# Performance work log

Hardware: AMD Instinct MI355X
Metric: run time of the kernel (lower is better)

Reference implementation:

```python
import jax, jax.numpy as jnp
import numpy as np

STRIDE = (4, 4)
MASK = (17, 17)
G_MEAN = 85.384
G_STD = 53.798
LEV = 5  # len(bins)
EPS = 1e-8
_BINS = np.array([0.0, 0.5, G_MEAN - G_STD, G_MEAN, G_MEAN + G_STD], dtype=np.float32)
_DISTS = [1, 2, 4]
_THETAS = [0.0, np.pi / 4, np.pi / 2, 3 * np.pi / 4]
# skimage greycomatrix offsets: (row, col) = (round(sin(t)*d), round(cos(t)*d)), dist-major
OFFSETS = [(int(round(np.sin(t) * d)), int(round(np.cos(t) * d))) for d in _DISTS for t in _THETAS]


def setup_inputs():
    key = jax.random.key(0)
    x = jax.random.uniform(key, (8, 1, 512, 512), dtype=jnp.float32) * 255.0
    return {"inputs": x}


def _sliding_windows(x):
    B, C, H, W = x.shape
    nx = (H - MASK[0]) // STRIDE[0] + 1
    ny = (W - MASK[1]) // STRIDE[1] + 1
    rows = (jnp.arange(nx) * STRIDE[0])[:, None] + jnp.arange(MASK[0])  # (nx, Mx)
    cols = (jnp.arange(ny) * STRIDE[1])[:, None] + jnp.arange(MASK[1])  # (ny, My)
    w = x[:, :, rows]              # (B, C, nx, Mx, W)
    w = w[:, :, :, :, cols]        # (B, C, nx, Mx, ny, My)
    return jnp.transpose(w, (0, 1, 2, 4, 3, 5))  # (B, C, nx, ny, Mx, My)


def _statistics(w):
    m = w.mean(axis=(-2, -1))
    s = w.std(axis=(-2, -1))
    mx = w.max(axis=(-2, -1))
    mn = w.min(axis=(-2, -1))
    # Faithful to original: mean is rescaled in-place BEFORE being used in max/min stats
    m = m / G_MEAN
    s = s / G_STD
    mx = (mx - m) / G_STD
    mn = (m - mn) / G_STD
    return jnp.concatenate([m, s, mx, mn], axis=1)  # (B, 4*C, nx, ny)


def _glcm(qf, dr, dc):
    # qf: (Wn, Mx, My) int32 -> normalized symmetric GLCM (Wn, LEV, LEV)
    Mx, My = qf.shape[-2:]
    if dc >= 0:
        a = qf[:, :Mx - dr, :My - dc]
        b = qf[:, dr:, dc:]
    else:
        a = qf[:, :Mx - dr, -dc:]
        b = qf[:, dr:, :My + dc]
    Wn = qf.shape[0]
    code = (a * LEV + b).reshape(Wn, -1)
    flat = (jnp.arange(Wn, dtype=jnp.int32)[:, None] * (LEV * LEV) + code).reshape(-1)
    cnt = jax.ops.segment_sum(jnp.ones(flat.shape, jnp.float32), flat, num_segments=Wn * LEV * LEV)
    G = cnt.reshape(Wn, LEV, LEV)
    G = G + jnp.swapaxes(G, -1, -2)  # symmetric=True
    return G / jnp.sum(G, axis=(-2, -1), keepdims=True)  # normed=True


def _hist_glcm_features(q):
    # q: (B, C, nx, ny, Mx, My) int32 -> (B, 64, nx, ny) (C must be 1)
    B, C, nx, ny, Mx, My = q.shape
    qf = q.reshape(-1, Mx, My)
    Wn = qf.shape[0]
    G = jnp.stack([_glcm(qf, dr, dc) for dr, dc in OFFSETS], axis=1)  # (Wn, 12, L, L)

    I = jnp.arange(LEV, dtype=jnp.float32)
    d2 = (I[:, None] - I[None, :]) ** 2
    contrast = jnp.einsum('wkij,ij->wk', G, d2)
    homogeneity = jnp.einsum('wkij,ij->wk', G, 1.0 / (1.0 + d2))
    energy = jnp.sqrt(jnp.sum(G * G, axis=(-2, -1)))
    Pi = G.sum(axis=-1)   # (Wn, 12, L)
    Pj = G.sum(axis=-2)
    mu_i = jnp.sum(I * Pi, axis=-1)
    mu_j = jnp.sum(I * Pj, axis=-1)
    di = I[None, None, :] - mu_i[..., None]
    dj = I[None, None, :] - mu_j[..., None]
    std_i = jnp.sqrt(jnp.sum(Pi * di * di, axis=-1))
    std_j = jnp.sqrt(jnp.sum(Pj * dj * dj, axis=-1))
    cov = jnp.einsum('wkij,wki,wkj->wk', G, di, dj)
    denom = std_i * std_j
    correlation = jnp.where(denom < 1e-15, 1.0, cov / jnp.maximum(denom, 1e-30))
    entropy = -jnp.sum(G * jnp.log2(G + EPS), axis=(-2, -1))  # (Wn, 12)

    qv = qf.reshape(Wn, -1)
    cnts = jnp.stack([jnp.sum(qv == k, axis=-1) for k in range(1, LEV)], axis=-1).astype(jnp.float32)
    tot = cnts.sum(axis=-1, keepdims=True)
    hist = jnp.where(tot > 0, cnts / jnp.maximum(tot, 1.0), 0.0)  # (Wn, LEV-1)

    feat = jnp.concatenate([hist, contrast, homogeneity, energy, correlation, entropy], axis=-1)
    feat = feat.reshape(B, C, nx, ny, -1)
    return jnp.transpose(feat, (0, 4, 2, 3, 1))[..., 0]  # (B, 64, nx, ny)


def reference(inputs):
    w = _sliding_windows(inputs)                                   # (B,C,nx,ny,17,17)
    stat = _statistics(w)                                          # (B,4,nx,ny)
    q = (jnp.digitize(w, jnp.asarray(_BINS)) - 1).astype(jnp.int32)
    hg = _hist_glcm_features(q)                                    # (B,64,nx,ny)
    feats = jnp.concatenate([stat, hg], axis=1)                    # (B,68,nx,ny)
    return jnp.mean(feats, axis=(-2, -1))                          # (B,68)
```

## Files before the change

kernel.cpp:

```cpp
#include <hip/hip_runtime.h>


#define G_MEAN_F 85.384f
#define G_STD_F  53.798f
#define MASK_WS_BYTES (8u * 512u * 36u * 8u)

__device__ constexpr int LO15[15] = {0,0,0,0,0,1,1,1,1,2,2,2,3,3,4};
__device__ constexpr int HI15[15] = {0,1,2,3,4,1,2,3,4,2,3,4,3,4,4};

__device__ __forceinline__ float wred(float v) {
#pragma unroll
  for (int m = 32; m; m >>= 1) v += __shfl_xor(v, m, 64);
  return v;
}

__device__ __forceinline__ void load_row(const unsigned long long* mrow, int ly4, unsigned m[5]) {
  unsigned long long a = mrow[0], b = mrow[1], c = mrow[2], d = mrow[3];
  m[1] = (unsigned)(a >> ly4) & 0x1FFFFu;
  m[2] = (unsigned)(b >> ly4) & 0x1FFFFu;
  m[3] = (unsigned)(c >> ly4) & 0x1FFFFu;
  m[4] = (unsigned)(d >> ly4) & 0x1FFFFu;
  m[0] = 0x1FFFFu & ~(m[1] | m[2] | m[3] | m[4]);
}

template<int DC>
__device__ __forceinline__ void updoff(unsigned cnt[15], const unsigned a[5], const unsigned b[5]) {
  unsigned as[5], bs[5];
#pragma unroll
  for (int v = 0; v < 5; ++v) {
    as[v] = (DC < 0) ? (a[v] >> (-DC)) : a[v];
    bs[v] = (DC > 0) ? (b[v] >> DC) : b[v];
  }
#pragma unroll
  for (int u = 0; u < 15; ++u) {
    const int i = LO15[u], j = HI15[u];
    unsigned t = as[i] & bs[j];
    if (i != j) t |= as[j] & bs[i];
    cnt[u] += __popc(t);
  }
}

__device__ __forceinline__ void feat5(const unsigned cnt[15], float Np,
                                      float& con, float& hom, float& ene,
                                      float& corr, float& ent) {
  const float invN = 1.0f / Np;
  const float inv2N = 0.5f / Np;
  con = 0.0f; hom = 0.0f; ent = 0.0f;
  float eac = 0.0f;
  float P[5] = {0, 0, 0, 0, 0};
#pragma unroll
  for (int u = 0; u < 15; ++u) {
    const int lo = LO15[u], hi = HI15[u];
    const float m = (float)cnt[u];
    const float d2 = (float)((hi - lo) * (hi - lo));
    con += m * d2;
    hom += m * (1.0f / (1.0f + d2));
    if (lo == hi) {
      eac += m * m;
      P[lo] += 2.0f * m;
      float g = m * invN;
      ent -= g * __log2f(g + 1e-8f);
    } else {
      eac += 0.5f * m * m;
      P[lo] += m; P[hi] += m;
      float g = m * inv2N;
      ent -= 2.0f * g * __log2f(g + 1e-8f);
    }
  }
  con *= invN;
  hom *= invN;
  ene = sqrtf(eac) * invN;
  float mu = 0.0f;
#pragma unroll
  for (int i = 0; i < 5; ++i) { P[i] *= inv2N; mu += (float)i * P[i]; }
  float s2 = 0.0f;
#pragma unroll
  for (int i = 0; i < 5; ++i) { float d = (float)i - mu; s2 = fmaf(P[i] * d, d, s2); }
  float denom = s2;
  float cov = 0.0f;
#pragma unroll
  for (int u = 0; u < 15; ++u)
    cov += ((float)cnt[u] * invN) * ((float)LO15[u] - mu) * ((float)HI15[u] - mu);
  corr = (denom < 1e-15f) ? 1.0f : cov / fmaxf(denom, 1e-30f);
}

__device__ __forceinline__ void emit2(const unsigned c1[15], const unsigned c2[15], float Np,
                                      bool v1, bool v2, float* pt0, int k0, int k1) {
  float con1, hom1, ene1, cor1, ent1, con2, hom2, ene2, cor2, ent2;
  feat5(c1, Np, con1, hom1, ene1, cor1, ent1);
  feat5(c2, Np, con2, hom2, ene2, cor2, ent2);
  if (!v1) { con1 = 0; hom1 = 0; ene1 = 0; cor1 = 0; ent1 = 0; }
  if (!v2) { con2 = 0; hom2 = 0; ene2 = 0; cor2 = 0; ent2 = 0; }
  float con = wred(con1 + con2), hom = wred(hom1 + hom2), ene = wred(ene1 + ene2);
  float cor = wred(cor1 + cor2), ent = wred(ent1 + ent2);
  if ((threadIdx.x & 63) == 0) {
    const float s = 1.0f / 15376.0f;
    pt0[(8 + k0) * 128] = con * s;
    pt0[(20 + k0) * 128] = hom * s;
    pt0[(32 + k0) * 128] = ene * s;
    pt0[(44 + k0) * 128] = cor * s;
    pt0[(56 + k0) * 128] = ent * s;
    if (k1 >= 0) {
      pt0[(8 + k1) * 128] = con * s;
      pt0[(20 + k1) * 128] = hom * s;
      pt0[(32 + k1) * 128] = ene * s;
      pt0[(44 + k1) * 128] = cor * s;
      pt0[(56 + k1) * 128] = ent * s;
    }
  }
}

template<int DR>
__device__ __forceinline__ void shiftbuf(unsigned buf[][5], const unsigned c[5]) {
#pragma unroll
  for (int i = 0; i < DR - 1; ++i)
#pragma unroll
    for (int v = 0; v < 5; ++v) buf[i][v] = buf[i + 1][v];
#pragma unroll
  for (int v = 0; v < 5; ++v) buf[DR - 1][v] = c[v];
}

template<int DR, int DC>
__device__ __forceinline__ void glcm_pass(const unsigned long long* mk, int s, int ly4,
                                          float Np, bool v1, bool v2, float* pt0,
                                          int k0, int k1) {
  unsigned A[15], S[15], B[15];
#pragma unroll
  for (int u = 0; u < 15; ++u) { A[u] = 0; S[u] = 0; B[u] = 0; }
  unsigned c[5];
  if (DR == 0) {
#pragma unroll 1
    for (int R = 0; R < 4; ++R)  { load_row(mk + (s + R) * 5, ly4, c); updoff<DC>(A, c, c); }
#pragma unroll 1
    for (int R = 4; R < 17; ++R) { load_row(mk + (s + R) * 5, ly4, c); updoff<DC>(S, c, c); }
#pragma unroll 1
    for (int R = 17; R < 21; ++R){ load_row(mk + (s + R) * 5, ly4, c); updoff<DC>(B, c, c); }
  } else {
    unsigned buf[DR > 0 ? DR : 1][5];
#pragma unroll
    for (int i = 0; i < DR; ++i) load_row(mk + (s + i) * 5, ly4, buf[i]);
#pragma unroll 1
    for (int R = 0; R < 4; ++R) {
      load_row(mk + (s + R + DR) * 5, ly4, c);
      updoff<DC>(A, buf[0], c);
      shiftbuf<DR>(buf, c);
    }
#pragma unroll 1
    for (int R = 4; R < 17 - DR; ++R) {
      load_row(mk + (s + R + DR) * 5, ly4, c);
      updoff<DC>(S, buf[0], c);
      shiftbuf<DR>(buf, c);
    }
#pragma unroll 1
    for (int R = 17 - DR; R < 21 - DR; ++R) {
      load_row(mk + (s + R + DR) * 5, ly4, c);
      updoff<DC>(B, buf[0], c);
      shiftbuf<DR>(buf, c);
    }
  }
#pragma unroll
  for (int u = 0; u < 15; ++u) { A[u] += S[u]; B[u] += S[u]; }
  emit2(A, B, Np, v1, v2, pt0, k0, k1);
}

__global__ __launch_bounds__(64)
void mask_build_kernel(const float* __restrict__ x, unsigned long long* __restrict__ mg) {
  const int lane = threadIdx.x;
  const int r = blockIdx.x;
  const int b = blockIdx.y;
  const float* xr = x + ((size_t)b * 512 + r) * 512;
  unsigned long long* mr = mg + ((size_t)b * 512 + r) * 36;

  const float T1 = 0.5f;
  const float T2 = (float)(85.384 - 53.798);
  const float T3 = 85.384f;
  const float T4 = (float)(85.384 + 53.798);

#pragma unroll 1
  for (int seg = 0; seg < 8; ++seg) {
    float xv = xr[seg * 64 + lane];
    int q = (int)(xv >= T1) + (int)(xv >= T2) + (int)(xv >= T3) + (int)(xv >= T4);
    unsigned long long b1 = __ballot(q == 1);
    unsigned long long b2 = __ballot(q == 2);
    unsigned long long b3 = __ballot(q == 3);
    unsigned long long b4 = __ballot(q == 4);
    if (lane < 4) {
      unsigned long long bv = (lane == 0) ? b1 : (lane == 1) ? b2 : (lane == 2) ? b3 : b4;
      mr[seg * 4 + lane] = bv;
    }
  }
  if (lane < 4) mr[32 + lane] = 0;
}

__global__ __launch_bounds__(128)
void glcm_feat_kernel(const float* __restrict__ x,
                      const unsigned long long* __restrict__ mg,
                      float* __restrict__ part) {
  __shared__ unsigned long long masks[77 * 5];

  const int tid = threadIdx.x;
  const int lane = tid & 63;
  const int wid = tid >> 6;
  const int u = blockIdx.x >> 4;
  const int ty = blockIdx.x & 15;
  const int tx = blockIdx.y;
  const int b = blockIdx.z;
  const int px0 = tx * 64;
  const int py0 = ty * 32;
  const float* xb = x + (size_t)b * 512 * 512;

  const int s0 = py0 >> 6;
  const int sh = py0 & 63;
  const unsigned long long* mgb = mg + (size_t)b * 512 * 36;
#pragma unroll 1
  for (int t = tid; t < 77 * 4; t += 128) {
    int row = t >> 2, lev = t & 3;
    int gr = px0 + row; if (gr > 511) gr = 511;
    const unsigned long long* p = mgb + (size_t)gr * 36 + s0 * 4 + lev;
    unsigned long long w0 = p[0];
    unsigned long long w1 = p[4];
    masks[row * 5 + lev] = sh ? ((w0 >> 32) | (w1 << 32)) : w0;
  }
  __syncthreads();

  const int lxp = lane >> 3, ly = lane & 7;
  const int wx1 = tx * 16 + 2 * lxp;
  const int wy = ty * 8 + ly;
  const bool vy = (wy < 124);
  const bool v1 = (wx1 < 124) && vy;
  const bool v2 = (wx1 + 1 < 124) && vy;
  const int s = 8 * lxp;
  const int ly4 = ly * 4;
  const int tile = tx * 16 + ty;
  float* pt0 = part + (size_t)b * 68 * 128 + tile;

  if (u == 0) {
    if (wid == 0) {
      int sp = px0 + s; if (sp > 488) sp = 488;
      int c0 = py0 + ly4; if (c0 > 492) c0 = 492;
      const float* fw = xb + (size_t)sp * 512 + c0;
      float sA = 0, qA = 0, sS = 0, qS = 0, sB = 0, qB = 0;
      float mxA = -1e30f, mnA = 1e30f, mxS = -1e30f, mnS = 1e30f, mxB = -1e30f, mnB = 1e30f;
#pragma unroll 1
      for (int r = 0; r < 21; ++r) {
        const float* p = fw + r * 512;
        const float4* p4 = (const float4*)p;
        float rs = 0, rq = 0, rmx = -1e30f, rmn = 1e30f;
#pragma unroll
        for (int w = 0; w < 4; ++w) {
          float4 f = p4[w];
          rs += f.x; rq = fmaf(f.x, f.x, rq); rmx = fmaxf(rmx, f.x); rmn = fminf(rmn, f.x);
          rs += f.y; rq = fmaf(f.y, f.y, rq); rmx = fmaxf(rmx, f.y); rmn = fminf(rmn, f.y);
          rs += f.z; rq = fmaf(f.z, f.z, rq); rmx = fmaxf(rmx, f.z); rmn = fminf(rmn, f.z);
          rs += f.w; rq = fmaf(f.w, f.w, rq); rmx = fmaxf(rmx, f.w); rmn = fminf(rmn, f.w);
        }
        float t = p[16];
        rs += t; rq = fmaf(t, t, rq); rmx = fmaxf(rmx, t); rmn = fminf(rmn, t);
        if (r < 4)       { sA += rs; qA += rq; mxA = fmaxf(mxA, rmx); mnA = fminf(mnA, rmn); }
        else if (r < 17) { sS += rs; qS += rq; mxS = fmaxf(mxS, rmx); mnS = fminf(mnS, rmn); }
        else             { sB += rs; qB += rq; mxB = fmaxf(mxB, rmx); mnB = fminf(mnB, rmn); }
      }
      float ch[4][2];
#pragma unroll
      for (int w = 0; w < 2; ++w) {
        float sum = w ? (sS + sB) : (sA + sS);
        float ssq = w ? (qS + qB) : (qA + qS);
        float mx = w ? fmaxf(mxS, mxB) : fmaxf(mxA, mxS);
        float mn = w ? fminf(mnS, mnB) : fminf(mnA, mnS);
        float mean = sum * (1.0f / 289.0f);
        float var = fmaxf(ssq * (1.0f / 289.0f) - mean * mean, 0.0f);
        float fm = mean / G_MEAN_F;
        ch[0][w] = fm;
        ch[1][w] = sqrtf(var) / G_STD_F;
        ch[2][w] = (mx - fm) / G_STD_F;
        ch[3][w] = (fm - mn) / G_STD_F;
      }
#pragma unroll
      for (int c = 0; c < 4; ++c) {
        float f = (v1 ? ch[c][0] : 0.0f) + (v2 ? ch[c][1] : 0.0f);
        f = wred(f);
        if (lane == 0) pt0[c * 128] = f * (1.0f / 15376.0f);
      }
    } else {
      unsigned hA[4] = {0,0,0,0}, hS[4] = {0,0,0,0}, hB[4] = {0,0,0,0};
#pragma unroll 1
      for (int R = 0; R < 21; ++R) {
        unsigned m[5];
        load_row(masks + (s + R) * 5, ly4, m);
        unsigned* h = (R < 4) ? hA : (R < 17) ? hS : hB;
#pragma unroll
        for (int v = 0; v < 4; ++v) h[v] += __popc(m[v + 1]);
      }
      float ch[4][2];
#pragma unroll
      for (int w = 0; w < 2; ++w) {
        unsigned t1 = w ? (hS[0] + hB[0]) : (hA[0] + hS[0]);
        unsigned t2 = w ? (hS[1] + hB[1]) : (hA[1] + hS[1]);
        unsigned t3 = w ? (hS[2] + hB[2]) : (hA[2] + hS[2]);
        unsigned t4 = w ? (hS[3] + hB[3]) : (hA[3] + hS[3]);
        unsigned tot = t1 + t2 + t3 + t4;
        float ti = (tot > 0) ? 1.0f / (float)tot : 0.0f;
        ch[0][w] = (float)t1 * ti;
        ch[1][w] = (float)t2 * ti;
        ch[2][w] = (float)t3 * ti;
        ch[3][w] = (float)t4 * ti;
      }
#pragma unroll
      for (int c = 0; c < 4; ++c) {
        float f = (v1 ? ch[c][0] : 0.0f) + (v2 ? ch[c][1] : 0.0f);
        f = wred(f);
        if (lane == 0) pt0[(4 + c) * 128] = f * (1.0f / 15376.0f);
      }
    }
  } else if (u == 1) {
    if (wid == 0) glcm_pass<0, 1>(masks, s, ly4, 272.0f, v1, v2, pt0, 0, -1);
    else          glcm_pass<1, 0>(masks, s, ly4, 272.0f, v1, v2, pt0, 2, -1);
  } else if (u == 2) {
    if (wid == 0) glcm_pass<0, 2>(masks, s, ly4, 255.0f, v1, v2, pt0, 4, -1);
    else          glcm_pass<1, 1>(masks, s, ly4, 256.0f, v1, v2, pt0, 1, 5);
  } else if (u == 3) {
    if (wid == 0) glcm_pass<0, 4>(masks, s, ly4, 221.0f, v1, v2, pt0, 8, -1);
    else          glcm_pass<1, -1>(masks, s, ly4, 256.0f, v1, v2, pt0, 3, 7);
  } else if (u == 4) {
    if (wid == 0) glcm_pass<2, 0>(masks, s, ly4, 255.0f, v1, v2, pt0, 6, -1);
    else          glcm_pass<3, 3>(masks, s, ly4, 196.0f, v1, v2, pt0, 9, -1);
  } else {
    if (wid == 0) glcm_pass<4, 0>(masks, s, ly4, 221.0f, v1, v2, pt0, 10, -1);
    else          glcm_pass<3, -3>(masks, s, ly4, 196.0f, v1, v2, pt0, 11, -1);
  }
}

__global__ __launch_bounds__(64)
void reduce_kernel(const float* __restrict__ part, float* __restrict__ out) {
  const int ch = blockIdx.x;
  const int b = blockIdx.y;
  const int lane = threadIdx.x;
  const float2* p = (const float2*)(part + ((size_t)b * 68 + ch) * 128);
  float2 f = p[lane];
  float v = f.x + f.y;
  v = wred(v);
  if (lane == 0) out[b * 68 + ch] = v;
}

extern "C" void kernel_launch(void* const* d_in, const int* in_sizes, int n_in,
                              void* d_out, int out_size, void* d_ws, size_t ws_size,
                              hipStream_t stream)
{
  const float* x = (const float*)d_in[0];
  float* out = (float*)d_out;
  unsigned long long* mg = (unsigned long long*)d_ws;
  float* part = (float*)((char*)d_ws + MASK_WS_BYTES);

  mask_build_kernel<<<dim3(512, 8), dim3(64), 0, stream>>>(x, mg);
  glcm_feat_kernel<<<dim3(96, 8, 8), dim3(128), 0, stream>>>(x, mg, part);
  reduce_kernel<<<dim3(68, 8), dim3(64), 0, stream>>>(part, out);
}
```

Baseline: 113.4 us.

## Process four vertically adjacent windows per thread with segmented row sharing

Each thread now covers four overlapping windows instead of two. Rows are split into seven segments whose partial GLCM counts, histograms and statistics are combined, so rows shared between windows are scanned once. Mask rows are pre-shifted into 17-bit shared-memory slices and read with a single uint4 load, which drops the per-row 64-bit shifts. The tile height doubles and the grid's x-tiles halve, which raises register pressure from the 7x15 counters and leaves fewer blocks in flight.

```diff
diff --git a/kernel.cpp b/kernel.cpp
--- a/kernel.cpp
+++ b/kernel.cpp
@@ -14,17 +14,14 @@
   return v;
 }
 
-__device__ __forceinline__ void load_row(const unsigned long long* mrow, int ly4, unsigned m[5]) {
-  unsigned long long a = mrow[0], b = mrow[1], c = mrow[2], d = mrow[3];
-  m[1] = (unsigned)(a >> ly4) & 0x1FFFFu;
-  m[2] = (unsigned)(b >> ly4) & 0x1FFFFu;
-  m[3] = (unsigned)(c >> ly4) & 0x1FFFFu;
-  m[4] = (unsigned)(d >> ly4) & 0x1FFFFu;
+__device__ __forceinline__ void load_sl(const unsigned* sl, int idx, unsigned m[5]) {
+  const uint4 q = *(const uint4*)(sl + idx * 4);
+  m[1] = q.x; m[2] = q.y; m[3] = q.z; m[4] = q.w;
   m[0] = 0x1FFFFu & ~(m[1] | m[2] | m[3] | m[4]);
 }
 
 template<int DC>
-__device__ __forceinline__ void updoff(unsigned cnt[15], const unsigned a[5], const unsigned b[5]) {
+__device__ __forceinline__ void updoff(unsigned* cnt, const unsigned a[5], const unsigned b[5]) {
   unsigned as[5], bs[5];
 #pragma unroll
   for (int v = 0; v < 5; ++v) {
@@ -40,7 +37,28 @@
   }
 }
 
-__device__ __forceinline__ void feat5(const unsigned cnt[15], float Np,
+template<int DR, int DC>
+__device__ __forceinline__ void seg_run(unsigned* cnt, const unsigned* sl, int sly,
+                                        int RB, int RE, unsigned (*buf)[5]) {
+#pragma unroll 1
+  for (int R = RB; R < RE; ++R) {
+    unsigned c[5];
+    load_sl(sl, sly + (R + DR) * 8, c);
+    if constexpr (DR > 0) {
+      updoff<DC>(cnt, buf[0], c);
+#pragma unroll
+      for (int i = 0; i < DR - 1; ++i)
+#pragma unroll
+        for (int v = 0; v < 5; ++v) buf[i][v] = buf[i + 1][v];
+#pragma unroll
+      for (int v = 0; v < 5; ++v) buf[DR - 1][v] = c[v];
+    } else {
+      updoff<DC>(cnt, c, c);
+    }
+  }
+}
+
+__device__ __forceinline__ void feat5(const unsigned* cnt, float Np,
                                       float& con, float& hom, float& ene,
                                       float& corr, float& ent) {
   const float invN = 1.0f / Np;
@@ -84,83 +102,89 @@
   corr = (denom < 1e-15f) ? 1.0f : cov / fmaxf(denom, 1e-30f);
 }
 
-__device__ __forceinline__ void emit2(const unsigned c1[15], const unsigned c2[15], float Np,
-                                      bool v1, bool v2, float* pt0, int k0, int k1) {
-  float con1, hom1, ene1, cor1, ent1, con2, hom2, ene2, cor2, ent2;
-  feat5(c1, Np, con1, hom1, ene1, cor1, ent1);
-  feat5(c2, Np, con2, hom2, ene2, cor2, ent2);
-  if (!v1) { con1 = 0; hom1 = 0; ene1 = 0; cor1 = 0; ent1 = 0; }
-  if (!v2) { con2 = 0; hom2 = 0; ene2 = 0; cor2 = 0; ent2 = 0; }
-  float con = wred(con1 + con2), hom = wred(hom1 + hom2), ene = wred(ene1 + ene2);
-  float cor = wred(cor1 + cor2), ent = wred(ent1 + ent2);
+template<int DR, int DC>
+__device__ void glcm4(const unsigned* sl, int sly, bool v0, bool v1, bool v2, bool v3,
+                      float Np, float* pt0, int k0, int k1) {
+  unsigned A[7][15];
+#pragma unroll
+  for (int p = 0; p < 7; ++p)
+#pragma unroll
+    for (int u = 0; u < 15; ++u) A[p][u] = 0;
+
+  unsigned buf[DR > 0 ? DR : 1][5];
+  if constexpr (DR > 0) {
+#pragma unroll
+    for (int i = 0; i < DR; ++i) load_sl(sl, sly + i * 8, buf[i]);
+  }
+  seg_run<DR, DC>(A[0], sl, sly, 0, 4, buf);
+  seg_run<DR, DC>(A[1], sl, sly, 4, 8, buf);
+  seg_run<DR, DC>(A[2], sl, sly, 8, 12, buf);
+  seg_run<DR, DC>(A[3], sl, sly, 12, 17 - DR, buf);
+  seg_run<DR, DC>(A[4], sl, sly, 17 - DR, 21 - DR, buf);
+  seg_run<DR, DC>(A[5], sl, sly, 21 - DR, 25 - DR, buf);
+  seg_run<DR, DC>(A[6], sl, sly, 25 - DR, 29 - DR, buf);
+
+#pragma unroll
+  for (int u = 0; u < 15; ++u) {
+    A[0][u] += A[1][u] + A[2][u] + A[3][u];
+    A[1][u] += A[2][u] + A[3][u] + A[4][u];
+    A[2][u] += A[3][u] + A[4][u] + A[5][u];
+    A[3][u] += A[4][u] + A[5][u] + A[6][u];
+  }
+  float con = 0, hom = 0, ene = 0, cor = 0, ent = 0;
+  const bool vv[4] = {v0, v1, v2, v3};
+#pragma unroll
+  for (int w = 0; w < 4; ++w) {
+    float c5, h5, e5, r5, t5;
+    feat5(A[w], Np, c5, h5, e5, r5, t5);
+    if (vv[w]) { con += c5; hom += h5; ene += e5; cor += r5; ent += t5; }
+  }
+  con = wred(con); hom = wred(hom); ene = wred(ene); cor = wred(cor); ent = wred(ent);
   if ((threadIdx.x & 63) == 0) {
     const float s = 1.0f / 15376.0f;
-    pt0[(8 + k0) * 128] = con * s;
-    pt0[(20 + k0) * 128] = hom * s;
-    pt0[(32 + k0) * 128] = ene * s;
-    pt0[(44 + k0) * 128] = cor * s;
-    pt0[(56 + k0) * 128] = ent * s;
+    pt0[(8 + k0) * 64] = con * s;
+    pt0[(20 + k0) * 64] = hom * s;
+    pt0[(32 + k0) * 64] = ene * s;
+    pt0[(44 + k0) * 64] = cor * s;
+    pt0[(56 + k0) * 64] = ent * s;
     if (k1 >= 0) {
-      pt0[(8 + k1) * 128] = con * s;
-      pt0[(20 + k1) * 128] = hom * s;
-      pt0[(32 + k1) * 128] = ene * s;
-      pt0[(44 + k1) * 128] = cor * s;
-      pt0[(56 + k1) * 128] = ent * s;
-    }
-  }
-}
-
-template<int DR>
-__device__ __forceinline__ void shiftbuf(unsigned buf[][5], const unsigned c[5]) {
-#pragma unroll
-  for (int i = 0; i < DR - 1; ++i)
-#pragma unroll
-    for (int v = 0; v < 5; ++v) buf[i][v] = buf[i + 1][v];
-#pragma unroll
-  for (int v = 0; v < 5; ++v) buf[DR - 1][v] = c[v];
-}
-
-template<int DR, int DC>
-__device__ __forceinline__ void glcm_pass(const unsigned long long* mk, int s, int ly4,
-                                          float Np, bool v1, bool v2, float* pt0,
-                                          int k0, int k1) {
-  unsigned A[15], S[15], B[15];
-#pragma unroll
-  for (int u = 0; u < 15; ++u) { A[u] = 0; S[u] = 0; B[u] = 0; }
-  unsigned c[5];
-  if (DR == 0) {
-#pragma unroll 1
-    for (int R = 0; R < 4; ++R)  { load_row(mk + (s + R) * 5, ly4, c); updoff<DC>(A, c, c); }
-#pragma unroll 1
-    for (int R = 4; R < 17; ++R) { load_row(mk + (s + R) * 5, ly4, c); updoff<DC>(S, c, c); }
-#pragma unroll 1
-    for (int R = 17; R < 21; ++R){ load_row(mk + (s + R) * 5, ly4, c); updoff<DC>(B, c, c); }
-  } else {
-    unsigned buf[DR > 0 ? DR : 1][5];
-#pragma unroll
-    for (int i = 0; i < DR; ++i) load_row(mk + (s + i) * 5, ly4, buf[i]);
-#pragma unroll 1
-    for (int R = 0; R < 4; ++R) {
-      load_row(mk + (s + R + DR) * 5, ly4, c);
-      updoff<DC>(A, buf[0], c);
-      shiftbuf<DR>(buf, c);
-    }
-#pragma unroll 1
-    for (int R = 4; R < 17 - DR; ++R) {
-      load_row(mk + (s + R + DR) * 5, ly4, c);
-      updoff<DC>(S, buf[0], c);
-      shiftbuf<DR>(buf, c);
-    }
-#pragma unroll 1
-    for (int R = 17 - DR; R < 21 - DR; ++R) {
-      load_row(mk + (s + R + DR) * 5, ly4, c);
-      updoff<DC>(B, buf[0], c);
-      shiftbuf<DR>(buf, c);
-    }
-  }
-#pragma unroll
-  for (int u = 0; u < 15; ++u) { A[u] += S[u]; B[u] += S[u]; }
-  emit2(A, B, Np, v1, v2, pt0, k0, k1);
+      pt0[(8 + k1) * 64] = con * s;
+      pt0[(20 + k1) * 64] = hom * s;
+      pt0[(32 + k1) * 64] = ene * s;
+      pt0[(44 + k1) * 64] = cor * s;
+      pt0[(56 + k1) * 64] = ent * s;
+    }
+  }
+}
+
+__device__ __forceinline__ void stat_rows(const float* fw, int RB, int RE,
+                                          float& sm, float& sq, float& mx, float& mn) {
+#pragma unroll 1
+  for (int r = RB; r < RE; ++r) {
+    const float* p = fw + r * 512;
+    const float4* p4 = (const float4*)p;
+    float rs = 0, rq = 0, rmx = -1e30f, rmn = 1e30f;
+#pragma unroll
+    for (int w = 0; w < 4; ++w) {
+      float4 f = p4[w];
+      rs += f.x; rq = fmaf(f.x, f.x, rq); rmx = fmaxf(rmx, f.x); rmn = fminf(rmn, f.x);
+      rs += f.y; rq = fmaf(f.y, f.y, rq); rmx = fmaxf(rmx, f.y); rmn = fminf(rmn, f.y);
+      rs += f.z; rq = fmaf(f.z, f.z, rq); rmx = fmaxf(rmx, f.z); rmn = fminf(rmn, f.z);
+      rs += f.w; rq = fmaf(f.w, f.w, rq); rmx = fmaxf(rmx, f.w); rmn = fminf(rmn, f.w);
+    }
+    float t = p[16];
+    rs += t; rq = fmaf(t, t, rq); rmx = fmaxf(rmx, t); rmn = fminf(rmn, t);
+    sm += rs; sq += rq; mx = fmaxf(mx, rmx); mn = fminf(mn, rmn);
+  }
+}
+
+__device__ __forceinline__ void hist_rows(const unsigned* sl, int sly, int RB, int RE,
+                                          unsigned* h) {
+#pragma unroll 1
+  for (int R = RB; R < RE; ++R) {
+    const uint4 q = *(const uint4*)(sl + (sly + R * 8) * 4);
+    h[0] += __popc(q.x); h[1] += __popc(q.y); h[2] += __popc(q.z); h[3] += __popc(q.w);
+  }
 }
 
 __global__ __launch_bounds__(64)
@@ -196,7 +220,7 @@
 void glcm_feat_kernel(const float* __restrict__ x,
                       const unsigned long long* __restrict__ mg,
                       float* __restrict__ part) {
-  __shared__ unsigned long long masks[77 * 5];
+  __shared__ __align__(16) unsigned sl[141 * 8 * 4];
 
   const int tid = threadIdx.x;
   const int lane = tid & 63;
@@ -205,128 +229,129 @@
   const int ty = blockIdx.x & 15;
   const int tx = blockIdx.y;
   const int b = blockIdx.z;
-  const int px0 = tx * 64;
+  const int px0 = tx * 128;
   const int py0 = ty * 32;
   const float* xb = x + (size_t)b * 512 * 512;
 
   const int s0 = py0 >> 6;
   const int sh = py0 & 63;
-  const unsigned long long* mgb = mg + (size_t)b * 512 * 36;
-#pragma unroll 1
-  for (int t = tid; t < 77 * 4; t += 128) {
-    int row = t >> 2, lev = t & 3;
+  const unsigned long long* mgb = mg + (size_t)b * 512 * 36 + s0 * 4;
+#pragma unroll 1
+  for (int t = tid; t < 141 * 8; t += 128) {
+    const int row = t >> 3, ly = t & 7;
     int gr = px0 + row; if (gr > 511) gr = 511;
-    const unsigned long long* p = mgb + (size_t)gr * 36 + s0 * 4 + lev;
-    unsigned long long w0 = p[0];
-    unsigned long long w1 = p[4];
-    masks[row * 5 + lev] = sh ? ((w0 >> 32) | (w1 << 32)) : w0;
+    const unsigned long long* p = mgb + (size_t)gr * 36;
+    unsigned sv[4];
+#pragma unroll
+    for (int lev = 0; lev < 4; ++lev) {
+      unsigned long long cmb = p[lev];
+      if (sh) cmb = (cmb >> 32) | (p[4 + lev] << 32);
+      sv[lev] = (unsigned)(cmb >> (4 * ly)) & 0x1FFFFu;
+    }
+    *(uint4*)(sl + t * 4) = make_uint4(sv[0], sv[1], sv[2], sv[3]);
   }
   __syncthreads();
 
   const int lxp = lane >> 3, ly = lane & 7;
-  const int wx1 = tx * 16 + 2 * lxp;
+  const int wxb = tx * 32 + 4 * lxp;
   const int wy = ty * 8 + ly;
   const bool vy = (wy < 124);
-  const bool v1 = (wx1 < 124) && vy;
-  const bool v2 = (wx1 + 1 < 124) && vy;
-  const int s = 8 * lxp;
-  const int ly4 = ly * 4;
+  const bool v0 = vy && (wxb < 124);
+  const bool v1 = vy && (wxb + 1 < 124);
+  const bool v2 = vy && (wxb + 2 < 124);
+  const bool v3 = vy && (wxb + 3 < 124);
+  const int s = 16 * lxp;
+  const int sly = s * 8 + ly;
   const int tile = tx * 16 + ty;
-  float* pt0 = part + (size_t)b * 68 * 128 + tile;
+  float* pt0 = part + (size_t)b * 68 * 64 + tile;
 
   if (u == 0) {
     if (wid == 0) {
-      int sp = px0 + s; if (sp > 488) sp = 488;
-      int c0 = py0 + ly4; if (c0 > 492) c0 = 492;
+      int sp = px0 + s; if (sp > 483) sp = 483;
+      int c0 = py0 + 4 * ly; if (c0 > 492) c0 = 492;
       const float* fw = xb + (size_t)sp * 512 + c0;
-      float sA = 0, qA = 0, sS = 0, qS = 0, sB = 0, qB = 0;
-      float mxA = -1e30f, mnA = 1e30f, mxS = -1e30f, mnS = 1e30f, mxB = -1e30f, mnB = 1e30f;
-#pragma unroll 1
-      for (int r = 0; r < 21; ++r) {
-        const float* p = fw + r * 512;
-        const float4* p4 = (const float4*)p;
-        float rs = 0, rq = 0, rmx = -1e30f, rmn = 1e30f;
-#pragma unroll
-        for (int w = 0; w < 4; ++w) {
-          float4 f = p4[w];
-          rs += f.x; rq = fmaf(f.x, f.x, rq); rmx = fmaxf(rmx, f.x); rmn = fminf(rmn, f.x);
-          rs += f.y; rq = fmaf(f.y, f.y, rq); rmx = fmaxf(rmx, f.y); rmn = fminf(rmn, f.y);
-          rs += f.z; rq = fmaf(f.z, f.z, rq); rmx = fmaxf(rmx, f.z); rmn = fminf(rmn, f.z);
-          rs += f.w; rq = fmaf(f.w, f.w, rq); rmx = fmaxf(rmx, f.w); rmn = fminf(rmn, f.w);
-        }
-        float t = p[16];
-        rs += t; rq = fmaf(t, t, rq); rmx = fmaxf(rmx, t); rmn = fminf(rmn, t);
-        if (r < 4)       { sA += rs; qA += rq; mxA = fmaxf(mxA, rmx); mnA = fminf(mnA, rmn); }
-        else if (r < 17) { sS += rs; qS += rq; mxS = fmaxf(mxS, rmx); mnS = fminf(mnS, rmn); }
-        else             { sB += rs; qB += rq; mxB = fmaxf(mxB, rmx); mnB = fminf(mnB, rmn); }
-      }
-      float ch[4][2];
-#pragma unroll
-      for (int w = 0; w < 2; ++w) {
-        float sum = w ? (sS + sB) : (sA + sS);
-        float ssq = w ? (qS + qB) : (qA + qS);
-        float mx = w ? fmaxf(mxS, mxB) : fmaxf(mxA, mxS);
-        float mn = w ? fminf(mnS, mnB) : fminf(mnA, mnS);
+      float sm[7], sq[7], mx[7], mn[7];
+#pragma unroll
+      for (int p = 0; p < 7; ++p) { sm[p] = 0; sq[p] = 0; mx[p] = -1e30f; mn[p] = 1e30f; }
+      stat_rows(fw, 0, 4, sm[0], sq[0], mx[0], mn[0]);
+      stat_rows(fw, 4, 8, sm[1], sq[1], mx[1], mn[1]);
+      stat_rows(fw, 8, 12, sm[2], sq[2], mx[2], mn[2]);
+      stat_rows(fw, 12, 17, sm[3], sq[3], mx[3], mn[3]);
+      stat_rows(fw, 17, 21, sm[4], sq[4], mx[4], mn[4]);
+      stat_rows(fw, 21, 25, sm[5], sq[5], mx[5], mn[5]);
+      stat_rows(fw, 25, 29, sm[6], sq[6], mx[6], mn[6]);
+      const bool vv[4] = {v0, v1, v2, v3};
+      float ch[4] = {0, 0, 0, 0};
+#pragma unroll
+      for (int w = 0; w < 4; ++w) {
+        float sum = sm[w] + sm[w + 1] + sm[w + 2] + sm[w + 3];
+        float ssq = sq[w] + sq[w + 1] + sq[w + 2] + sq[w + 3];
+        float wmx = fmaxf(fmaxf(mx[w], mx[w + 1]), fmaxf(mx[w + 2], mx[w + 3]));
+        float wmn = fminf(fminf(mn[w], mn[w + 1]), fminf(mn[w + 2], mn[w + 3]));
         float mean = sum * (1.0f / 289.0f);
         float var = fmaxf(ssq * (1.0f / 289.0f) - mean * mean, 0.0f);
         float fm = mean / G_MEAN_F;
-        ch[0][w] = fm;
-        ch[1][w] = sqrtf(var) / G_STD_F;
-        ch[2][w] = (mx - fm) / G_STD_F;
-        ch[3][w] = (fm - mn) / G_STD_F;
+        if (vv[w]) {
+          ch[0] += fm;
+          ch[1] += sqrtf(var) / G_STD_F;
+          ch[2] += (wmx - fm) / G_STD_F;
+          ch[3] += (fm - wmn) / G_STD_F;
+        }
       }
 #pragma unroll
       for (int c = 0; c < 4; ++c) {
-        float f = (v1 ? ch[c][0] : 0.0f) + (v2 ? ch[c][1] : 0.0f);
-        f = wred(f);
-        if (lane == 0) pt0[c * 128] = f * (1.0f / 15376.0f);
+        float f = wred(ch[c]);
+        if (lane == 0) pt0[c * 64] = f * (1.0f / 15376.0f);
       }
     } else {
-      unsigned hA[4] = {0,0,0,0}, hS[4] = {0,0,0,0}, hB[4] = {0,0,0,0};
-#pragma unroll 1
-      for (int R = 0; R < 21; ++R) {
-        unsigned m[5];
-        load_row(masks + (s + R) * 5, ly4, m);
-        unsigned* h = (R < 4) ? hA : (R < 17) ? hS : hB;
-#pragma unroll
-        for (int v = 0; v < 4; ++v) h[v] += __popc(m[v + 1]);
-      }
-      float ch[4][2];
-#pragma unroll
-      for (int w = 0; w < 2; ++w) {
-        unsigned t1 = w ? (hS[0] + hB[0]) : (hA[0] + hS[0]);
-        unsigned t2 = w ? (hS[1] + hB[1]) : (hA[1] + hS[1]);
-        unsigned t3 = w ? (hS[2] + hB[2]) : (hA[2] + hS[2]);
-        unsigned t4 = w ? (hS[3] + hB[3]) : (hA[3] + hS[3]);
+      unsigned hh[7][4];
+#pragma unroll
+      for (int p = 0; p < 7; ++p) { hh[p][0] = 0; hh[p][1] = 0; hh[p][2] = 0; hh[p][3] = 0; }
+      hist_rows(sl, sly, 0, 4, hh[0]);
+      hist_rows(sl, sly, 4, 8, hh[1]);
+      hist_rows(sl, sly, 8, 12, hh[2]);
+      hist_rows(sl, sly, 12, 17, hh[3]);
+      hist_rows(sl, sly, 17, 21, hh[4]);
+      hist_rows(sl, sly, 21, 25, hh[5]);
+      hist_rows(sl, sly, 25, 29, hh[6]);
+      const bool vv[4] = {v0, v1, v2, v3};
+      float ch[4] = {0, 0, 0, 0};
+#pragma unroll
+      for (int w = 0; w < 4; ++w) {
+        unsigned t1 = hh[w][0] + hh[w + 1][0] + hh[w + 2][0] + hh[w + 3][0];
+        unsigned t2 = hh[w][1] + hh[w + 1][1] + hh[w + 2][1] + hh[w + 3][1];
+        unsigned t3 = hh[w][2] + hh[w + 1][2] + hh[w + 2][2] + hh[w + 3][2];
+        unsigned t4 = hh[w][3] + hh[w + 1][3] + hh[w + 2][3] + hh[w + 3][3];
         unsigned tot = t1 + t2 + t3 + t4;
         float ti = (tot > 0) ? 1.0f / (float)tot : 0.0f;
-        ch[0][w] = (float)t1 * ti;
-        ch[1][w] = (float)t2 * ti;
-        ch[2][w] = (float)t3 * ti;
-        ch[3][w] = (float)t4 * ti;
+        if (vv[w]) {
+          ch[0] += (float)t1 * ti;
+          ch[1] += (float)t2 * ti;
+          ch[2] += (float)t3 * ti;
+          ch[3] += (float)t4 * ti;
+        }
       }
 #pragma unroll
       for (int c = 0; c < 4; ++c) {
-        float f = (v1 ? ch[c][0] : 0.0f) + (v2 ? ch[c][1] : 0.0f);
-        f = wred(f);
-        if (lane == 0) pt0[(4 + c) * 128] = f * (1.0f / 15376.0f);
+        float f = wred(ch[c]);
+        if (lane == 0) pt0[(4 + c) * 64] = f * (1.0f / 15376.0f);
       }
     }
   } else if (u == 1) {
-    if (wid == 0) glcm_pass<0, 1>(masks, s, ly4, 272.0f, v1, v2, pt0, 0, -1);
-    else          glcm_pass<1, 0>(masks, s, ly4, 272.0f, v1, v2, pt0, 2, -1);
+    if (wid == 0) glcm4<0, 1>(sl, sly, v0, v1, v2, v3, 272.0f, pt0, 0, -1);
+    else          glcm4<1, 0>(sl, sly, v0, v1, v2, v3, 272.0f, pt0, 2, -1);
   } else if (u == 2) {
-    if (wid == 0) glcm_pass<0, 2>(masks, s, ly4, 255.0f, v1, v2, pt0, 4, -1);
-    else          glcm_pass<1, 1>(masks, s, ly4, 256.0f, v1, v2, pt0, 1, 5);
+    if (wid == 0) glcm4<0, 2>(sl, sly, v0, v1, v2, v3, 255.0f, pt0, 4, -1);
+    else          glcm4<1, 1>(sl, sly, v0, v1, v2, v3, 256.0f, pt0, 1, 5);
   } else if (u == 3) {
-    if (wid == 0) glcm_pass<0, 4>(masks, s, ly4, 221.0f, v1, v2, pt0, 8, -1);
-    else          glcm_pass<1, -1>(masks, s, ly4, 256.0f, v1, v2, pt0, 3, 7);
+    if (wid == 0) glcm4<0, 4>(sl, sly, v0, v1, v2, v3, 221.0f, pt0, 8, -1);
+    else          glcm4<1, -1>(sl, sly, v0, v1, v2, v3, 256.0f, pt0, 3, 7);
   } else if (u == 4) {
-    if (wid == 0) glcm_pass<2, 0>(masks, s, ly4, 255.0f, v1, v2, pt0, 6, -1);
-    else          glcm_pass<3, 3>(masks, s, ly4, 196.0f, v1, v2, pt0, 9, -1);
+    if (wid == 0) glcm4<2, 0>(sl, sly, v0, v1, v2, v3, 255.0f, pt0, 6, -1);
+    else          glcm4<3, 3>(sl, sly, v0, v1, v2, v3, 196.0f, pt0, 9, -1);
   } else {
-    if (wid == 0) glcm_pass<4, 0>(masks, s, ly4, 221.0f, v1, v2, pt0, 10, -1);
-    else          glcm_pass<3, -3>(masks, s, ly4, 196.0f, v1, v2, pt0, 11, -1);
+    if (wid == 0) glcm4<4, 0>(sl, sly, v0, v1, v2, v3, 221.0f, pt0, 10, -1);
+    else          glcm4<3, -3>(sl, sly, v0, v1, v2, v3, 196.0f, pt0, 11, -1);
   }
 }
 
@@ -335,9 +360,7 @@
   const int ch = blockIdx.x;
   const int b = blockIdx.y;
   const int lane = threadIdx.x;
-  const float2* p = (const float2*)(part + ((size_t)b * 68 + ch) * 128);
-  float2 f = p[lane];
-  float v = f.x + f.y;
+  float v = part[((size_t)b * 68 + ch) * 64 + lane];
   v = wred(v);
   if (lane == 0) out[b * 68 + ch] = v;
 }
@@ -352,6 +375,6 @@
   float* part = (float*)((char*)d_ws + MASK_WS_BYTES);
 
   mask_build_kernel<<<dim3(512, 8), dim3(64), 0, stream>>>(x, mg);
-  glcm_feat_kernel<<<dim3(96, 8, 8), dim3(128), 0, stream>>>(x, mg, part);
+  glcm_feat_kernel<<<dim3(96, 4, 8), dim3(128), 0, stream>>>(x, mg, part);
   reduce_kernel<<<dim3(68, 8), dim3(64), 0, stream>>>(part, out);
 }
```

Measured after the change: 119.0 us. +4.9%, slower.

## Merge per-offset blocks into one 12-wave block with pre-sliced shared masks

Applied to the files above, without the earlier changes.

Each block previously handled one of six work groups (stats/hist or two GLCM offsets) per tile, so the shared mask staging was repeated six times per tile. Now a single 768-thread block per tile runs all twelve roles as separate wavefronts over one shared staging. The staging pre-extracts the 17-bit per-lane slices into a uint4 layout, which removes the per-row shift/mask work in the inner loops. The row loop also prefetches the next row. The cost is a grid that drops to 1024 large blocks and uneven per-wave work inside each block, which may reduce occupancy and load balance.

```diff
diff --git a/kernel.cpp b/kernel.cpp
--- a/kernel.cpp
+++ b/kernel.cpp
@@ -14,17 +14,14 @@
   return v;
 }
 
-__device__ __forceinline__ void load_row(const unsigned long long* mrow, int ly4, unsigned m[5]) {
-  unsigned long long a = mrow[0], b = mrow[1], c = mrow[2], d = mrow[3];
-  m[1] = (unsigned)(a >> ly4) & 0x1FFFFu;
-  m[2] = (unsigned)(b >> ly4) & 0x1FFFFu;
-  m[3] = (unsigned)(c >> ly4) & 0x1FFFFu;
-  m[4] = (unsigned)(d >> ly4) & 0x1FFFFu;
+__device__ __forceinline__ void load_sl(const unsigned* sl, int idx, unsigned m[5]) {
+  const uint4 q = *(const uint4*)(sl + idx * 4);
+  m[1] = q.x; m[2] = q.y; m[3] = q.z; m[4] = q.w;
   m[0] = 0x1FFFFu & ~(m[1] | m[2] | m[3] | m[4]);
 }
 
 template<int DC>
-__device__ __forceinline__ void updoff(unsigned cnt[15], const unsigned a[5], const unsigned b[5]) {
+__device__ __forceinline__ void updoff(unsigned* cnt, const unsigned a[5], const unsigned b[5]) {
   unsigned as[5], bs[5];
 #pragma unroll
   for (int v = 0; v < 5; ++v) {
@@ -40,7 +37,7 @@
   }
 }
 
-__device__ __forceinline__ void feat5(const unsigned cnt[15], float Np,
+__device__ __forceinline__ void feat5(const unsigned* cnt, float Np,
                                       float& con, float& hom, float& ene,
                                       float& corr, float& ent) {
   const float invN = 1.0f / Np;
@@ -110,54 +107,45 @@
   }
 }
 
-template<int DR>
-__device__ __forceinline__ void shiftbuf(unsigned buf[][5], const unsigned c[5]) {
-#pragma unroll
-  for (int i = 0; i < DR - 1; ++i)
-#pragma unroll
-    for (int v = 0; v < 5; ++v) buf[i][v] = buf[i + 1][v];
-#pragma unroll
-  for (int v = 0; v < 5; ++v) buf[DR - 1][v] = c[v];
-}
-
 template<int DR, int DC>
-__device__ __forceinline__ void glcm_pass(const unsigned long long* mk, int s, int ly4,
-                                          float Np, bool v1, bool v2, float* pt0,
-                                          int k0, int k1) {
+__device__ void glcm2(const unsigned* sl, int s, int ly, bool v1, bool v2,
+                      float Np, float* pt0, int k0, int k1) {
   unsigned A[15], S[15], B[15];
 #pragma unroll
   for (int u = 0; u < 15; ++u) { A[u] = 0; S[u] = 0; B[u] = 0; }
-  unsigned c[5];
-  if (DR == 0) {
-#pragma unroll 1
-    for (int R = 0; R < 4; ++R)  { load_row(mk + (s + R) * 5, ly4, c); updoff<DC>(A, c, c); }
-#pragma unroll 1
-    for (int R = 4; R < 17; ++R) { load_row(mk + (s + R) * 5, ly4, c); updoff<DC>(S, c, c); }
-#pragma unroll 1
-    for (int R = 17; R < 21; ++R){ load_row(mk + (s + R) * 5, ly4, c); updoff<DC>(B, c, c); }
-  } else {
-    unsigned buf[DR > 0 ? DR : 1][5];
-#pragma unroll
-    for (int i = 0; i < DR; ++i) load_row(mk + (s + i) * 5, ly4, buf[i]);
-#pragma unroll 1
-    for (int R = 0; R < 4; ++R) {
-      load_row(mk + (s + R + DR) * 5, ly4, c);
-      updoff<DC>(A, buf[0], c);
-      shiftbuf<DR>(buf, c);
-    }
-#pragma unroll 1
-    for (int R = 4; R < 17 - DR; ++R) {
-      load_row(mk + (s + R + DR) * 5, ly4, c);
-      updoff<DC>(S, buf[0], c);
-      shiftbuf<DR>(buf, c);
-    }
-#pragma unroll 1
-    for (int R = 17 - DR; R < 21 - DR; ++R) {
-      load_row(mk + (s + R + DR) * 5, ly4, c);
-      updoff<DC>(B, buf[0], c);
-      shiftbuf<DR>(buf, c);
-    }
-  }
+  unsigned buf[DR > 0 ? DR : 1][5];
+  if constexpr (DR > 0) {
+#pragma unroll
+    for (int i = 0; i < DR; ++i) load_sl(sl, (s + i) * 8 + ly, buf[i]);
+  }
+  unsigned nxt[5];
+  load_sl(sl, (s + DR) * 8 + ly, nxt);
+
+#define SEGRUN(CNT, RB, RE)                                              \
+  _Pragma("unroll 1")                                                    \
+  for (int R = (RB); R < (RE); ++R) {                                    \
+    unsigned cur[5];                                                     \
+    _Pragma("unroll")                                                    \
+    for (int v = 0; v < 5; ++v) cur[v] = nxt[v];                         \
+    load_sl(sl, (s + DR + R + 1) * 8 + ly, nxt);  \
+    if constexpr (DR > 0) {                                              \
+      updoff<DC>(CNT, buf[0], cur);                                      \
+      _Pragma("unroll")                                                  \
+      for (int i = 0; i < DR - 1; ++i)                                   \
+        _Pragma("unroll")                                                \
+        for (int v = 0; v < 5; ++v) buf[i][v] = buf[i + 1][v];           \
+      _Pragma("unroll")                                                  \
+      for (int v = 0; v < 5; ++v) buf[DR > 0 ? DR - 1 : 0][v] = cur[v];  \
+    } else {                                                             \
+      updoff<DC>(CNT, cur, cur);                                         \
+    }                                                                    \
+  }
+
+  SEGRUN(A, 0, 4)
+  SEGRUN(S, 4, 17 - DR)
+  SEGRUN(B, 17 - DR, 21 - DR)
+#undef SEGRUN
+
 #pragma unroll
   for (int u = 0; u < 15; ++u) { A[u] += S[u]; B[u] += S[u]; }
   emit2(A, B, Np, v1, v2, pt0, k0, k1);
@@ -192,17 +180,16 @@
   if (lane < 4) mr[32 + lane] = 0;
 }
 
-__global__ __launch_bounds__(128)
+__global__ __launch_bounds__(768)
 void glcm_feat_kernel(const float* __restrict__ x,
                       const unsigned long long* __restrict__ mg,
                       float* __restrict__ part) {
-  __shared__ unsigned long long masks[77 * 5];
+  __shared__ __align__(16) unsigned sl[79 * 8 * 4];
 
   const int tid = threadIdx.x;
   const int lane = tid & 63;
   const int wid = tid >> 6;
-  const int u = blockIdx.x >> 4;
-  const int ty = blockIdx.x & 15;
+  const int ty = blockIdx.x;
   const int tx = blockIdx.y;
   const int b = blockIdx.z;
   const int px0 = tx * 64;
@@ -211,15 +198,22 @@
 
   const int s0 = py0 >> 6;
   const int sh = py0 & 63;
-  const unsigned long long* mgb = mg + (size_t)b * 512 * 36;
+  const unsigned long long* mgb = mg + (size_t)b * 512 * 36 + s0 * 4;
 #pragma unroll 1
-  for (int t = tid; t < 77 * 4; t += 128) {
-    int row = t >> 2, lev = t & 3;
-    int gr = px0 + row; if (gr > 511) gr = 511;
-    const unsigned long long* p = mgb + (size_t)gr * 36 + s0 * 4 + lev;
-    unsigned long long w0 = p[0];
-    unsigned long long w1 = p[4];
-    masks[row * 5 + lev] = sh ? ((w0 >> 32) | (w1 << 32)) : w0;
+  for (int t = tid; t < 79 * 8; t += 768) {
+    const int row = t >> 3, ly = t & 7;
+    unsigned sv[4] = {0, 0, 0, 0};
+    if (row < 77) {
+      int gr = px0 + row; if (gr > 511) gr = 511;
+      const unsigned long long* p = mgb + (size_t)gr * 36;
+#pragma unroll
+      for (int lev = 0; lev < 4; ++lev) {
+        unsigned long long cmb = p[lev];
+        if (sh) cmb = (cmb >> 32) | (p[4 + lev] << 32);
+        sv[lev] = (unsigned)(cmb >> (4 * ly)) & 0x1FFFFu;
+      }
+    }
+    *(uint4*)(sl + t * 4) = make_uint4(sv[0], sv[1], sv[2], sv[3]);
   }
   __syncthreads();
 
@@ -230,103 +224,103 @@
   const bool v1 = (wx1 < 124) && vy;
   const bool v2 = (wx1 + 1 < 124) && vy;
   const int s = 8 * lxp;
-  const int ly4 = ly * 4;
   const int tile = tx * 16 + ty;
   float* pt0 = part + (size_t)b * 68 * 128 + tile;
 
-  if (u == 0) {
-    if (wid == 0) {
-      int sp = px0 + s; if (sp > 488) sp = 488;
-      int c0 = py0 + ly4; if (c0 > 492) c0 = 492;
-      const float* fw = xb + (size_t)sp * 512 + c0;
-      float sA = 0, qA = 0, sS = 0, qS = 0, sB = 0, qB = 0;
-      float mxA = -1e30f, mnA = 1e30f, mxS = -1e30f, mnS = 1e30f, mxB = -1e30f, mnB = 1e30f;
+  if (wid == 0) {
+    int sp = px0 + s; if (sp > 488) sp = 488;
+    int c0 = py0 + 4 * ly; if (c0 > 492) c0 = 492;
+    const float* fw = xb + (size_t)sp * 512 + c0;
+    float sA = 0, qA = 0, sS = 0, qS = 0, sB = 0, qB = 0;
+    float mxA = -1e30f, mnA = 1e30f, mxS = -1e30f, mnS = 1e30f, mxB = -1e30f, mnB = 1e30f;
 #pragma unroll 1
-      for (int r = 0; r < 21; ++r) {
-        const float* p = fw + r * 512;
-        const float4* p4 = (const float4*)p;
-        float rs = 0, rq = 0, rmx = -1e30f, rmn = 1e30f;
-#pragma unroll
-        for (int w = 0; w < 4; ++w) {
-          float4 f = p4[w];
-          rs += f.x; rq = fmaf(f.x, f.x, rq); rmx = fmaxf(rmx, f.x); rmn = fminf(rmn, f.x);
-          rs += f.y; rq = fmaf(f.y, f.y, rq); rmx = fmaxf(rmx, f.y); rmn = fminf(rmn, f.y);
-          rs += f.z; rq = fmaf(f.z, f.z, rq); rmx = fmaxf(rmx, f.z); rmn = fminf(rmn, f.z);
-          rs += f.w; rq = fmaf(f.w, f.w, rq); rmx = fmaxf(rmx, f.w); rmn = fminf(rmn, f.w);
-        }
-        float t = p[16];
-        rs += t; rq = fmaf(t, t, rq); rmx = fmaxf(rmx, t); rmn = fminf(rmn, t);
-        if (r < 4)       { sA += rs; qA += rq; mxA = fmaxf(mxA, rmx); mnA = fminf(mnA, rmn); }
-        else if (r < 17) { sS += rs; qS += rq; mxS = fmaxf(mxS, rmx); mnS = fminf(mnS, rmn); }
-        else             { sB += rs; qB += rq; mxB = fmaxf(mxB, rmx); mnB = fminf(mnB, rmn); }
+    for (int r = 0; r < 21; ++r) {
+      const float* p = fw + r * 512;
+      const float4* p4 = (const float4*)p;
+      float rs = 0, rq = 0, rmx = -1e30f, rmn = 1e30f;
+#pragma unroll
+      for (int w = 0; w < 4; ++w) {
+        float4 f = p4[w];
+        rs += f.x; rq = fmaf(f.x, f.x, rq); rmx = fmaxf(rmx, f.x); rmn = fminf(rmn, f.x);
+        rs += f.y; rq = fmaf(f.y, f.y, rq); rmx = fmaxf(rmx, f.y); rmn = fminf(rmn, f.y);
+        rs += f.z; rq = fmaf(f.z, f.z, rq); rmx = fmaxf(rmx, f.z); rmn = fminf(rmn, f.z);
+        rs += f.w; rq = fmaf(f.w, f.w, rq); rmx = fmaxf(rmx, f.w); rmn = fminf(rmn, f.w);
       }
-      float ch[4][2];
-#pragma unroll
-      for (int w = 0; w < 2; ++w) {
-        float sum = w ? (sS + sB) : (sA + sS);
-        float ssq = w ? (qS + qB) : (qA + qS);
-        float mx = w ? fmaxf(mxS, mxB) : fmaxf(mxA, mxS);
-        float mn = w ? fminf(mnS, mnB) : fminf(mnA, mnS);
-        float mean = sum * (1.0f / 289.0f);
-        float var = fmaxf(ssq * (1.0f / 289.0f) - mean * mean, 0.0f);
-        float fm = mean / G_MEAN_F;
-        ch[0][w] = fm;
-        ch[1][w] = sqrtf(var) / G_STD_F;
-        ch[2][w] = (mx - fm) / G_STD_F;
-        ch[3][w] = (fm - mn) / G_STD_F;
-      }
-#pragma unroll
-      for (int c = 0; c < 4; ++c) {
-        float f = (v1 ? ch[c][0] : 0.0f) + (v2 ? ch[c][1] : 0.0f);
-        f = wred(f);
-        if (lane == 0) pt0[c * 128] = f * (1.0f / 15376.0f);
-      }
-    } else {
-      unsigned hA[4] = {0,0,0,0}, hS[4] = {0,0,0,0}, hB[4] = {0,0,0,0};
+      float t = p[16];
+      rs += t; rq = fmaf(t, t, rq); rmx = fmaxf(rmx, t); rmn = fminf(rmn, t);
+      if (r < 4)       { sA += rs; qA += rq; mxA = fmaxf(mxA, rmx); mnA = fminf(mnA, rmn); }
+      else if (r < 17) { sS += rs; qS += rq; mxS = fmaxf(mxS, rmx); mnS = fminf(mnS, rmn); }
+      else             { sB += rs; qB += rq; mxB = fmaxf(mxB, rmx); mnB = fminf(mnB, rmn); }
+    }
+    float ch[4][2];
+#pragma unroll
+    for (int w = 0; w < 2; ++w) {
+      float sum = w ? (sS + sB) : (sA + sS);
+      float ssq = w ? (qS + qB) : (qA + qS);
+      float mx = w ? fmaxf(mxS, mxB) : fmaxf(mxA, mxS);
+      float mn = w ? fminf(mnS, mnB) : fminf(mnA, mnS);
+      float mean = sum * (1.0f / 289.0f);
+      float var = fmaxf(ssq * (1.0f / 289.0f) - mean * mean, 0.0f);
+      float fm = mean / G_MEAN_F;
+      ch[0][w] = fm;
+      ch[1][w] = sqrtf(var) / G_STD_F;
+      ch[2][w] = (mx - fm) / G_STD_F;
+      ch[3][w] = (fm - mn) / G_STD_F;
+    }
+#pragma unroll
+    for (int c = 0; c < 4; ++c) {
+      float f = (v1 ? ch[c][0] : 0.0f) + (v2 ? ch[c][1] : 0.0f);
+      f = wred(f);
+      if (lane == 0) pt0[c * 128] = f * (1.0f / 15376.0f);
+    }
+  } else if (wid == 1) {
+    unsigned hA[4] = {0,0,0,0}, hS[4] = {0,0,0,0}, hB[4] = {0,0,0,0};
 #pragma unroll 1
-      for (int R = 0; R < 21; ++R) {
-        unsigned m[5];
-        load_row(masks + (s + R) * 5, ly4, m);
-        unsigned* h = (R < 4) ? hA : (R < 17) ? hS : hB;
-#pragma unroll
-        for (int v = 0; v < 4; ++v) h[v] += __popc(m[v + 1]);
-      }
-      float ch[4][2];
-#pragma unroll
-      for (int w = 0; w < 2; ++w) {
-        unsigned t1 = w ? (hS[0] + hB[0]) : (hA[0] + hS[0]);
-        unsigned t2 = w ? (hS[1] + hB[1]) : (hA[1] + hS[1]);
-        unsigned t3 = w ? (hS[2] + hB[2]) : (hA[2] + hS[2]);
-        unsigned t4 = w ? (hS[3] + hB[3]) : (hA[3] + hS[3]);
-        unsigned tot = t1 + t2 + t3 + t4;
-        float ti = (tot > 0) ? 1.0f / (float)tot : 0.0f;
-        ch[0][w] = (float)t1 * ti;
-        ch[1][w] = (float)t2 * ti;
-        ch[2][w] = (float)t3 * ti;
-        ch[3][w] = (float)t4 * ti;
-      }
-#pragma unroll
-      for (int c = 0; c < 4; ++c) {
-        float f = (v1 ? ch[c][0] : 0.0f) + (v2 ? ch[c][1] : 0.0f);
-        f = wred(f);
-        if (lane == 0) pt0[(4 + c) * 128] = f * (1.0f / 15376.0f);
-      }
-    }
-  } else if (u == 1) {
-    if (wid == 0) glcm_pass<0, 1>(masks, s, ly4, 272.0f, v1, v2, pt0, 0, -1);
-    else          glcm_pass<1, 0>(masks, s, ly4, 272.0f, v1, v2, pt0, 2, -1);
-  } else if (u == 2) {
-    if (wid == 0) glcm_pass<0, 2>(masks, s, ly4, 255.0f, v1, v2, pt0, 4, -1);
-    else          glcm_pass<1, 1>(masks, s, ly4, 256.0f, v1, v2, pt0, 1, 5);
-  } else if (u == 3) {
-    if (wid == 0) glcm_pass<0, 4>(masks, s, ly4, 221.0f, v1, v2, pt0, 8, -1);
-    else          glcm_pass<1, -1>(masks, s, ly4, 256.0f, v1, v2, pt0, 3, 7);
-  } else if (u == 4) {
-    if (wid == 0) glcm_pass<2, 0>(masks, s, ly4, 255.0f, v1, v2, pt0, 6, -1);
-    else          glcm_pass<3, 3>(masks, s, ly4, 196.0f, v1, v2, pt0, 9, -1);
+    for (int R = 0; R < 21; ++R) {
+      const uint4 q = *(const uint4*)(sl + ((s + R) * 8 + ly) * 4);
+      unsigned* h = (R < 4) ? hA : (R < 17) ? hS : hB;
+      h[0] += __popc(q.x); h[1] += __popc(q.y); h[2] += __popc(q.z); h[3] += __popc(q.w);
+    }
+    float ch[4][2];
+#pragma unroll
+    for (int w = 0; w < 2; ++w) {
+      unsigned t1 = w ? (hS[0] + hB[0]) : (hA[0] + hS[0]);
+      unsigned t2 = w ? (hS[1] + hB[1]) : (hA[1] + hS[1]);
+      unsigned t3 = w ? (hS[2] + hB[2]) : (hA[2] + hS[2]);
+      unsigned t4 = w ? (hS[3] + hB[3]) : (hA[3] + hS[3]);
+      unsigned tot = t1 + t2 + t3 + t4;
+      float ti = (tot > 0) ? 1.0f / (float)tot : 0.0f;
+      ch[0][w] = (float)t1 * ti;
+      ch[1][w] = (float)t2 * ti;
+      ch[2][w] = (float)t3 * ti;
+      ch[3][w] = (float)t4 * ti;
+    }
+#pragma unroll
+    for (int c = 0; c < 4; ++c) {
+      float f = (v1 ? ch[c][0] : 0.0f) + (v2 ? ch[c][1] : 0.0f);
+      f = wred(f);
+      if (lane == 0) pt0[(4 + c) * 128] = f * (1.0f / 15376.0f);
+    }
+  } else if (wid == 2) {
+    glcm2<0, 1>(sl, s, ly, v1, v2, 272.0f, pt0, 0, -1);
+  } else if (wid == 3) {
+    glcm2<1, 0>(sl, s, ly, v1, v2, 272.0f, pt0, 2, -1);
+  } else if (wid == 4) {
+    glcm2<0, 2>(sl, s, ly, v1, v2, 255.0f, pt0, 4, -1);
+  } else if (wid == 5) {
+    glcm2<1, 1>(sl, s, ly, v1, v2, 256.0f, pt0, 1, 5);
+  } else if (wid == 6) {
+    glcm2<0, 4>(sl, s, ly, v1, v2, 221.0f, pt0, 8, -1);
+  } else if (wid == 7) {
+    glcm2<1, -1>(sl, s, ly, v1, v2, 256.0f, pt0, 3, 7);
+  } else if (wid == 8) {
+    glcm2<2, 0>(sl, s, ly, v1, v2, 255.0f, pt0, 6, -1);
+  } else if (wid == 9) {
+    glcm2<3, 3>(sl, s, ly, v1, v2, 196.0f, pt0, 9, -1);
+  } else if (wid == 10) {
+    glcm2<4, 0>(sl, s, ly, v1, v2, 221.0f, pt0, 10, -1);
   } else {
-    if (wid == 0) glcm_pass<4, 0>(masks, s, ly4, 221.0f, v1, v2, pt0, 10, -1);
-    else          glcm_pass<3, -3>(masks, s, ly4, 196.0f, v1, v2, pt0, 11, -1);
+    glcm2<3, -3>(sl, s, ly, v1, v2, 196.0f, pt0, 11, -1);
   }
 }
 
@@ -352,6 +346,6 @@
   float* part = (float*)((char*)d_ws + MASK_WS_BYTES);
 
   mask_build_kernel<<<dim3(512, 8), dim3(64), 0, stream>>>(x, mg);
-  glcm_feat_kernel<<<dim3(96, 8, 8), dim3(128), 0, stream>>>(x, mg, part);
+  glcm_feat_kernel<<<dim3(16, 8, 8), dim3(768), 0, stream>>>(x, mg, part);
   reduce_kernel<<<dim3(68, 8), dim3(64), 0, stream>>>(part, out);
 }
```

New measurement: 109.3 us, median of 2. 3.7% less time.
